# Kernel tuning notes

Hardware: AMD Instinct MI355X
Metric: run time of the kernel (lower is better)

The kernel has to match this reference:

```python
import jax, jax.numpy as jnp
import numpy as np


def setup_inputs() -> dict:
    key = jax.random.key(0)
    k1, k2 = jax.random.split(key)
    B, C, H, W = 128, 2, 256, 256
    inp = jax.random.normal(k1, (B, C, H, W), dtype=jnp.float32)
    tgt = jax.random.uniform(k2, (B, C, H, W), dtype=jnp.float32)
    return {"input": inp, "target": tgt}


def reference(input, target):
    B, C, H, W = input.shape
    f32 = jnp.float32
    # coordinate maps: y[p,:] = (p+1-H/2)/H, x[:,j] = (j+1-W/2)/W
    ys = ((jnp.arange(H, dtype=f32) + 1.0) - H / 2.0) / H          # [H]
    xs = ((jnp.arange(W, dtype=f32) + 1.0) - W / 2.0) / W          # [W]

    # per-heatmap softmax over flattened HxW (DSNT)
    p = jax.nn.softmax(input.reshape(B, C, H * W), axis=-1).reshape(B, C, H, W)
    pred_x = jnp.einsum('bchw,w->bc', p, xs)                        # [B,C]
    pred_y = jnp.einsum('bchw,h->bc', p, ys)                        # [B,C]

    # hard argmax on ground truth heatmaps (constant w.r.t. grads)
    idx = jnp.argmax(target.reshape(B, C, H * W), axis=-1)          # [B,C] int
    true_x = ((idx % W).astype(f32) + 1.0 - W / 2.0) / W
    true_y = ((idx // W).astype(f32) + 1.0 - H / 2.0) / H

    # euclidean distance loss per heatmap
    ed = jnp.sqrt((true_x - pred_x) ** 2 + (true_y - pred_y) ** 2)  # [B,C]

    # Jensen-Shannon divergence, faithful to the torch code:
    # kl(a, b) := KLDivLoss(input=a, target=b) = mean(b * (log(b) - a))
    m = 0.5 * (target + p)
    logm = jnp.log(m)
    kl_im = jnp.mean(m * (logm - target), axis=(-2, -1))            # kl(gt, m)
    kl_tm = jnp.mean(m * (logm - p), axis=(-2, -1))                 # kl(pred, m)
    jsd = 0.5 * kl_im + 0.5 * kl_tm                                 # [B,C]

    s = jnp.sum(ed + jsd)

    # inter-landmark distance term (channels 0 and 1)
    pred_dist = jnp.sqrt((pred_x[:, 0] - pred_x[:, 1]) ** 2 + (pred_y[:, 0] - pred_y[:, 1]) ** 2)
    true_dist = jnp.sqrt((true_x[:, 0] - true_x[:, 1]) ** 2 + (true_y[:, 0] - true_y[:, 1]) ** 2)
    diff_dist_abs = jnp.sqrt((pred_dist - true_dist) ** 2) / true_dist
    s = s + jnp.sum(diff_dist_abs)

    return (s / B).reshape(1)
```

## Files before the change

kernel.cpp:

```cpp
#include <hip/hip_runtime.h>
#include <math.h>

#define HM_H 256
#define HM_W 256
#define HM_N (HM_H * HM_W)
#define N_HM 256
#define NTHR 1024
#define NWAVES (NTHR / 64)
#define ITERS (HM_N / 4 / NTHR)


__global__ __launch_bounds__(NTHR) void heatmap_kernel(
    const float* __restrict__ inp, const float* __restrict__ tgt,
    float* __restrict__ ws)
{
    const int hm = blockIdx.x;
    const size_t base = (size_t)hm * HM_N;
    const float4* __restrict__ in4 = (const float4*)(inp + base);
    const float4* __restrict__ tg4 = (const float4*)(tgt + base);
    const int tid = threadIdx.x;

    float mval = -INFINITY, sacc = 0.0f;
    float bval = -INFINITY;
    int   bidx = HM_N;
#pragma unroll
    for (int it = 0; it < ITERS; ++it) {
        const int v = it * NTHR + tid;
        const float4 x = in4[v];
        const float4 t = tg4[v];
        const float lm = fmaxf(fmaxf(x.x, x.y), fmaxf(x.z, x.w));
        if (lm > mval) { sacc *= __expf(mval - lm); mval = lm; }
        sacc += __expf(x.x - mval) + __expf(x.y - mval)
              + __expf(x.z - mval) + __expf(x.w - mval);
        const int i0 = v * 4;
        if (t.x > bval) { bval = t.x; bidx = i0; }
        if (t.y > bval) { bval = t.y; bidx = i0 + 1; }
        if (t.z > bval) { bval = t.z; bidx = i0 + 2; }
        if (t.w > bval) { bval = t.w; bidx = i0 + 3; }
    }

#pragma unroll
    for (int off = 1; off < 64; off <<= 1) {
        const float m2 = __shfl_xor(mval, off);
        const float s2 = __shfl_xor(sacc, off);
        const float nm = fmaxf(mval, m2);
        sacc = sacc * __expf(mval - nm) + s2 * __expf(m2 - nm);
        mval = nm;
        const float bv2 = __shfl_xor(bval, off);
        const int   bi2 = __shfl_xor(bidx, off);
        if (bv2 > bval || (bv2 == bval && bi2 < bidx)) { bval = bv2; bidx = bi2; }
    }

    __shared__ float lm_[NWAVES], ls_[NWAVES], lbv_[NWAVES];
    __shared__ int   lbi_[NWAVES];
    __shared__ float s_max, s_invZ;
    __shared__ int   s_idx;
    const int wid = tid >> 6, lane = tid & 63;
    if (lane == 0) { lm_[wid] = mval; ls_[wid] = sacc; lbv_[wid] = bval; lbi_[wid] = bidx; }
    __syncthreads();
    if (tid == 0) {
        float M = lm_[0], S = ls_[0], BV = lbv_[0];
        int BI = lbi_[0];
        for (int i = 1; i < NWAVES; ++i) {
            const float m2 = lm_[i], s2 = ls_[i];
            const float nm = fmaxf(M, m2);
            S = S * __expf(M - nm) + s2 * __expf(m2 - nm);
            M = nm;
            if (lbv_[i] > BV || (lbv_[i] == BV && lbi_[i] < BI)) { BV = lbv_[i]; BI = lbi_[i]; }
        }
        s_max = M; s_invZ = 1.0f / S; s_idx = BI;
    }
    __syncthreads();
    const float gmax = s_max, ginvZ = s_invZ;

    float px = 0.0f, py = 0.0f, jsd = 0.0f;
    const float cscale = 1.0f / 256.0f;
#pragma unroll
    for (int it = 0; it < ITERS; ++it) {
        const int v = it * NTHR + tid;
        const float4 x = in4[v];
        const float4 t = tg4[v];
        const int i0 = v * 4;
        const float yh  = ((float)(i0 >> 8) + 1.0f - 128.0f) * cscale;
        const float xw0 = ((float)(i0 & 255) + 1.0f - 128.0f) * cscale;

        const float p0 = __expf(x.x - gmax) * ginvZ;
        const float p1 = __expf(x.y - gmax) * ginvZ;
        const float p2 = __expf(x.z - gmax) * ginvZ;
        const float p3 = __expf(x.w - gmax) * ginvZ;

        px += p0 * xw0 + p1 * (xw0 + cscale) + p2 * (xw0 + 2.0f * cscale)
            + p3 * (xw0 + 3.0f * cscale);
        py += (p0 + p1 + p2 + p3) * yh;

        const float m0 = 0.5f * (t.x + p0);
        const float m1 = 0.5f * (t.y + p1);
        const float m2 = 0.5f * (t.z + p2);
        const float m3 = 0.5f * (t.w + p3);
        jsd += m0 * (__logf(m0) - m0);
        jsd += m1 * (__logf(m1) - m1);
        jsd += m2 * (__logf(m2) - m2);
        jsd += m3 * (__logf(m3) - m3);
    }

#pragma unroll
    for (int off = 1; off < 64; off <<= 1) {
        px  += __shfl_xor(px, off);
        py  += __shfl_xor(py, off);
        jsd += __shfl_xor(jsd, off);
    }
    __shared__ float lpx[NWAVES], lpy[NWAVES], ljs[NWAVES];
    if (lane == 0) { lpx[wid] = px; lpy[wid] = py; ljs[wid] = jsd; }
    __syncthreads();
    if (tid == 0) {
        float PX = 0.0f, PY = 0.0f, JS = 0.0f;
        for (int i = 0; i < NWAVES; ++i) { PX += lpx[i]; PY += lpy[i]; JS += ljs[i]; }
        ws[hm]           = PX;
        ws[N_HM + hm]    = PY;
        ws[2 * N_HM + hm] = JS * (1.0f / (float)HM_N);
        const int bi = s_idx;
        ws[3 * N_HM + hm] = ((float)(bi & 255) + 1.0f - 128.0f) * (1.0f / 256.0f);
        ws[4 * N_HM + hm] = ((float)(bi >> 8)  + 1.0f - 128.0f) * (1.0f / 256.0f);
    }
}

__global__ __launch_bounds__(256) void finalize_kernel(
    const float* __restrict__ ws, float* __restrict__ out)
{
    __shared__ float acc[256];
    const int t = threadIdx.x;
    const float* px  = ws;
    const float* py  = ws + N_HM;
    const float* jsd = ws + 2 * N_HM;
    const float* tx  = ws + 3 * N_HM;
    const float* ty  = ws + 4 * N_HM;

    const float ex = tx[t] - px[t];
    const float ey = ty[t] - py[t];
    float v = sqrtf(ex * ex + ey * ey) + jsd[t];

    if (t < 128) {
        const int a = 2 * t, b = 2 * t + 1;
        const float pdx = px[a] - px[b], pdy = py[a] - py[b];
        const float pd  = sqrtf(pdx * pdx + pdy * pdy);
        const float tdx = tx[a] - tx[b], tdy = ty[a] - ty[b];
        const float td  = sqrtf(tdx * tdx + tdy * tdy);
        v += fabsf(pd - td) / td;
    }
    acc[t] = v;
    __syncthreads();
#pragma unroll
    for (int off = 128; off > 0; off >>= 1) {
        if (t < off) acc[t] += acc[t + off];
        __syncthreads();
    }
    if (t == 0) out[0] = acc[0] * (1.0f / 128.0f);
}

extern "C" void kernel_launch(void* const* d_in, const int* in_sizes, int n_in,
                              void* d_out, int out_size, void* d_ws, size_t ws_size,
                              hipStream_t stream) {
    const float* inp = (const float*)d_in[0];
    const float* tgt = (const float*)d_in[1];
    float* out = (float*)d_out;
    float* ws  = (float*)d_ws;

    heatmap_kernel<<<N_HM, NTHR, 0, stream>>>(inp, tgt, ws);
    finalize_kernel<<<1, 256, 0, stream>>>(ws, out);
}
```

Before: 164.4 us.

## Split each heatmap across eight blocks with separate sum-exp pass and packed argmax

Replaces the one-block-per-heatmap kernel with a sum-of-exp pass and a main pass, each using eight blocks per heatmap, with final reductions done in the finalize kernel. The softmax drops max subtraction, computing exp(x) directly. The argmax is packed as a 64-bit key for a cheap max reduction. This targets the low parallelism and serial per-heatmap work of the old kernel, at the cost of an extra kernel launch and a re-read of the input, and it risks overflow for large logits.

```diff
diff --git a/kernel.cpp b/kernel.cpp
--- a/kernel.cpp
+++ b/kernel.cpp
@@ -5,102 +5,114 @@
 #define HM_W 256
 #define HM_N (HM_H * HM_W)
 #define N_HM 256
-#define NTHR 1024
-#define NWAVES (NTHR / 64)
-#define ITERS (HM_N / 4 / NTHR)
-
-
-__global__ __launch_bounds__(NTHR) void heatmap_kernel(
+#define PARTS 8
+#define NPART (N_HM * PARTS)
+#define PIX_PART (HM_N / PARTS)
+#define NTHR 256
+#define F4T (PIX_PART / 4 / NTHR)
+
+#define WS_Z   0
+#define WS_PX  2048
+#define WS_PY  4096
+#define WS_JS  6144
+#define WS_PK  8192
+
+__global__ __launch_bounds__(NTHR, 8) void sumexp_kernel(
+    const float* __restrict__ inp, float* __restrict__ ws)
+{
+    const int part = blockIdx.x;
+    const float4* __restrict__ in4 =
+        (const float4*)(inp + (size_t)part * PIX_PART);
+    const int tid = threadIdx.x;
+
+    float4 v[F4T];
+#pragma unroll
+    for (int i = 0; i < F4T; ++i) v[i] = in4[i * NTHR + tid];
+
+    float s0 = 0.f, s1 = 0.f, s2 = 0.f, s3 = 0.f;
+#pragma unroll
+    for (int i = 0; i < F4T; ++i) {
+        s0 += __expf(v[i].x); s1 += __expf(v[i].y);
+        s2 += __expf(v[i].z); s3 += __expf(v[i].w);
+    }
+    float s = (s0 + s1) + (s2 + s3);
+#pragma unroll
+    for (int off = 1; off < 64; off <<= 1) s += __shfl_xor(s, off);
+
+    __shared__ float ls[NTHR / 64];
+    const int wid = tid >> 6, lane = tid & 63;
+    if (lane == 0) ls[wid] = s;
+    __syncthreads();
+    if (tid == 0) ws[WS_Z + part] = (ls[0] + ls[1]) + (ls[2] + ls[3]);
+}
+
+__global__ __launch_bounds__(NTHR, 4) void main_kernel(
     const float* __restrict__ inp, const float* __restrict__ tgt,
     float* __restrict__ ws)
 {
-    const int hm = blockIdx.x;
-    const size_t base = (size_t)hm * HM_N;
+    const int part = blockIdx.x;
+    const int hm = part >> 3;
+    const int tid = threadIdx.x;
+
+    float Z = 0.f;
+#pragma unroll
+    for (int i = 0; i < PARTS; ++i) Z += ws[WS_Z + hm * PARTS + i];
+    const float invZ = 1.0f / Z;
+
+    const size_t base = (size_t)part * PIX_PART;
     const float4* __restrict__ in4 = (const float4*)(inp + base);
     const float4* __restrict__ tg4 = (const float4*)(tgt + base);
-    const int tid = threadIdx.x;
-
-    float mval = -INFINITY, sacc = 0.0f;
-    float bval = -INFINITY;
-    int   bidx = HM_N;
-#pragma unroll
-    for (int it = 0; it < ITERS; ++it) {
-        const int v = it * NTHR + tid;
-        const float4 x = in4[v];
-        const float4 t = tg4[v];
-        const float lm = fmaxf(fmaxf(x.x, x.y), fmaxf(x.z, x.w));
-        if (lm > mval) { sacc *= __expf(mval - lm); mval = lm; }
-        sacc += __expf(x.x - mval) + __expf(x.y - mval)
-              + __expf(x.z - mval) + __expf(x.w - mval);
-        const int i0 = v * 4;
-        if (t.x > bval) { bval = t.x; bidx = i0; }
-        if (t.y > bval) { bval = t.y; bidx = i0 + 1; }
-        if (t.z > bval) { bval = t.z; bidx = i0 + 2; }
-        if (t.w > bval) { bval = t.w; bidx = i0 + 3; }
-    }
-
-#pragma unroll
-    for (int off = 1; off < 64; off <<= 1) {
-        const float m2 = __shfl_xor(mval, off);
-        const float s2 = __shfl_xor(sacc, off);
-        const float nm = fmaxf(mval, m2);
-        sacc = sacc * __expf(mval - nm) + s2 * __expf(m2 - nm);
-        mval = nm;
-        const float bv2 = __shfl_xor(bval, off);
-        const int   bi2 = __shfl_xor(bidx, off);
-        if (bv2 > bval || (bv2 == bval && bi2 < bidx)) { bval = bv2; bidx = bi2; }
-    }
-
-    __shared__ float lm_[NWAVES], ls_[NWAVES], lbv_[NWAVES];
-    __shared__ int   lbi_[NWAVES];
-    __shared__ float s_max, s_invZ;
-    __shared__ int   s_idx;
-    const int wid = tid >> 6, lane = tid & 63;
-    if (lane == 0) { lm_[wid] = mval; ls_[wid] = sacc; lbv_[wid] = bval; lbi_[wid] = bidx; }
-    __syncthreads();
-    if (tid == 0) {
-        float M = lm_[0], S = ls_[0], BV = lbv_[0];
-        int BI = lbi_[0];
-        for (int i = 1; i < NWAVES; ++i) {
-            const float m2 = lm_[i], s2 = ls_[i];
-            const float nm = fmaxf(M, m2);
-            S = S * __expf(M - nm) + s2 * __expf(m2 - nm);
-            M = nm;
-            if (lbv_[i] > BV || (lbv_[i] == BV && lbi_[i] < BI)) { BV = lbv_[i]; BI = lbi_[i]; }
+    const int pix0 = (part & (PARTS - 1)) * PIX_PART;
+
+    const float cs = 1.0f / 256.0f;
+    float px = 0.f, py = 0.f, jsd = 0.f;
+    unsigned long long best = 0ull;
+
+#pragma unroll
+    for (int half = 0; half < 2; ++half) {
+        float4 x[4], t[4];
+#pragma unroll
+        for (int i = 0; i < 4; ++i) {
+            const int f4 = (half * 4 + i) * NTHR + tid;
+            x[i] = in4[f4];
+            t[i] = tg4[f4];
         }
-        s_max = M; s_invZ = 1.0f / S; s_idx = BI;
-    }
-    __syncthreads();
-    const float gmax = s_max, ginvZ = s_invZ;
-
-    float px = 0.0f, py = 0.0f, jsd = 0.0f;
-    const float cscale = 1.0f / 256.0f;
-#pragma unroll
-    for (int it = 0; it < ITERS; ++it) {
-        const int v = it * NTHR + tid;
-        const float4 x = in4[v];
-        const float4 t = tg4[v];
-        const int i0 = v * 4;
-        const float yh  = ((float)(i0 >> 8) + 1.0f - 128.0f) * cscale;
-        const float xw0 = ((float)(i0 & 255) + 1.0f - 128.0f) * cscale;
-
-        const float p0 = __expf(x.x - gmax) * ginvZ;
-        const float p1 = __expf(x.y - gmax) * ginvZ;
-        const float p2 = __expf(x.z - gmax) * ginvZ;
-        const float p3 = __expf(x.w - gmax) * ginvZ;
-
-        px += p0 * xw0 + p1 * (xw0 + cscale) + p2 * (xw0 + 2.0f * cscale)
-            + p3 * (xw0 + 3.0f * cscale);
-        py += (p0 + p1 + p2 + p3) * yh;
-
-        const float m0 = 0.5f * (t.x + p0);
-        const float m1 = 0.5f * (t.y + p1);
-        const float m2 = 0.5f * (t.z + p2);
-        const float m3 = 0.5f * (t.w + p3);
-        jsd += m0 * (__logf(m0) - m0);
-        jsd += m1 * (__logf(m1) - m1);
-        jsd += m2 * (__logf(m2) - m2);
-        jsd += m3 * (__logf(m3) - m3);
+#pragma unroll
+        for (int i = 0; i < 4; ++i) {
+            const int f4 = (half * 4 + i) * NTHR + tid;
+            const int gp = pix0 + f4 * 4;
+            const float yh  = ((float)(gp >> 8) + 1.0f - 128.0f) * cs;
+            const float xw0 = ((float)(gp & 255) + 1.0f - 128.0f) * cs;
+
+            const float p0 = __expf(x[i].x) * invZ;
+            const float p1 = __expf(x[i].y) * invZ;
+            const float p2 = __expf(x[i].z) * invZ;
+            const float p3 = __expf(x[i].w) * invZ;
+
+            px += p0 * xw0 + p1 * (xw0 + cs) + p2 * (xw0 + 2.f * cs)
+                + p3 * (xw0 + 3.f * cs);
+            py += ((p0 + p1) + (p2 + p3)) * yh;
+
+            const float m0 = 0.5f * (t[i].x + p0);
+            const float m1 = 0.5f * (t[i].y + p1);
+            const float m2 = 0.5f * (t[i].z + p2);
+            const float m3 = 0.5f * (t[i].w + p3);
+            jsd += m0 * (__logf(m0) - m0) + m1 * (__logf(m1) - m1)
+                 + m2 * (__logf(m2) - m2) + m3 * (__logf(m3) - m3);
+
+            const unsigned long long k0 =
+                ((unsigned long long)__float_as_uint(t[i].x) << 32) | (unsigned)(65535 - gp);
+            const unsigned long long k1 =
+                ((unsigned long long)__float_as_uint(t[i].y) << 32) | (unsigned)(65534 - gp);
+            const unsigned long long k2 =
+                ((unsigned long long)__float_as_uint(t[i].z) << 32) | (unsigned)(65533 - gp);
+            const unsigned long long k3 =
+                ((unsigned long long)__float_as_uint(t[i].w) << 32) | (unsigned)(65532 - gp);
+            unsigned long long ka = k0 > k1 ? k0 : k1;
+            unsigned long long kb = k2 > k3 ? k2 : k3;
+            ka = ka > kb ? ka : kb;
+            best = best > ka ? best : ka;
+        }
     }
 
 #pragma unroll
@@ -108,42 +120,62 @@
         px  += __shfl_xor(px, off);
         py  += __shfl_xor(py, off);
         jsd += __shfl_xor(jsd, off);
-    }
-    __shared__ float lpx[NWAVES], lpy[NWAVES], ljs[NWAVES];
-    if (lane == 0) { lpx[wid] = px; lpy[wid] = py; ljs[wid] = jsd; }
+        const unsigned long long b2 = __shfl_xor(best, off);
+        best = best > b2 ? best : b2;
+    }
+
+    __shared__ float lpx[4], lpy[4], ljs[4];
+    __shared__ unsigned long long lbk[4];
+    const int wid = tid >> 6, lane = tid & 63;
+    if (lane == 0) { lpx[wid] = px; lpy[wid] = py; ljs[wid] = jsd; lbk[wid] = best; }
     __syncthreads();
     if (tid == 0) {
-        float PX = 0.0f, PY = 0.0f, JS = 0.0f;
-        for (int i = 0; i < NWAVES; ++i) { PX += lpx[i]; PY += lpy[i]; JS += ljs[i]; }
-        ws[hm]           = PX;
-        ws[N_HM + hm]    = PY;
-        ws[2 * N_HM + hm] = JS * (1.0f / (float)HM_N);
-        const int bi = s_idx;
-        ws[3 * N_HM + hm] = ((float)(bi & 255) + 1.0f - 128.0f) * (1.0f / 256.0f);
-        ws[4 * N_HM + hm] = ((float)(bi >> 8)  + 1.0f - 128.0f) * (1.0f / 256.0f);
+        float PX = 0.f, PY = 0.f, JS = 0.f;
+        unsigned long long BK = 0ull;
+        for (int i = 0; i < 4; ++i) {
+            PX += lpx[i]; PY += lpy[i]; JS += ljs[i];
+            BK = BK > lbk[i] ? BK : lbk[i];
+        }
+        ws[WS_PX + part] = PX;
+        ws[WS_PY + part] = PY;
+        ws[WS_JS + part] = JS;
+        ((unsigned long long*)(ws + WS_PK))[part] = BK;
     }
 }
 
 __global__ __launch_bounds__(256) void finalize_kernel(
     const float* __restrict__ ws, float* __restrict__ out)
 {
-    __shared__ float acc[256];
     const int t = threadIdx.x;
-    const float* px  = ws;
-    const float* py  = ws + N_HM;
-    const float* jsd = ws + 2 * N_HM;
-    const float* tx  = ws + 3 * N_HM;
-    const float* ty  = ws + 4 * N_HM;
-
-    const float ex = tx[t] - px[t];
-    const float ey = ty[t] - py[t];
-    float v = sqrtf(ex * ex + ey * ey) + jsd[t];
+    const unsigned long long* packp = (const unsigned long long*)(ws + WS_PK);
+
+    float PX = 0.f, PY = 0.f, JS = 0.f;
+    unsigned long long BK = 0ull;
+#pragma unroll
+    for (int i = 0; i < PARTS; ++i) {
+        PX += ws[WS_PX + t * PARTS + i];
+        PY += ws[WS_PY + t * PARTS + i];
+        JS += ws[WS_JS + t * PARTS + i];
+        const unsigned long long b = packp[t * PARTS + i];
+        BK = BK > b ? BK : b;
+    }
+    JS *= (1.0f / (float)HM_N);
+    const int gp = 65535 - (int)(BK & 0xFFFFFFFFull);
+    const float tx = ((float)(gp & 255) + 1.0f - 128.0f) * (1.0f / 256.0f);
+    const float ty = ((float)(gp >> 8)  + 1.0f - 128.0f) * (1.0f / 256.0f);
+
+    const float ex = tx - PX, ey = ty - PY;
+    float v = sqrtf(ex * ex + ey * ey) + JS;
+
+    __shared__ float sPX[256], sPY[256], sTX[256], sTY[256], acc[256];
+    sPX[t] = PX; sPY[t] = PY; sTX[t] = tx; sTY[t] = ty;
+    __syncthreads();
 
     if (t < 128) {
         const int a = 2 * t, b = 2 * t + 1;
-        const float pdx = px[a] - px[b], pdy = py[a] - py[b];
+        const float pdx = sPX[a] - sPX[b], pdy = sPY[a] - sPY[b];
         const float pd  = sqrtf(pdx * pdx + pdy * pdy);
-        const float tdx = tx[a] - tx[b], tdy = ty[a] - ty[b];
+        const float tdx = sTX[a] - sTX[b], tdy = sTY[a] - sTY[b];
         const float td  = sqrtf(tdx * tdx + tdy * tdy);
         v += fabsf(pd - td) / td;
     }
@@ -165,6 +197,7 @@
     float* out = (float*)d_out;
     float* ws  = (float*)d_ws;
 
-    heatmap_kernel<<<N_HM, NTHR, 0, stream>>>(inp, tgt, ws);
+    sumexp_kernel<<<NPART, NTHR, 0, stream>>>(inp, ws);
+    main_kernel<<<NPART, NTHR, 0, stream>>>(inp, tgt, ws);
     finalize_kernel<<<1, 256, 0, stream>>>(ws, out);
 }
```

Result: faster. 150.5 us (-8.5%).
